# Performance work log

Measured on AMD Instinct MI355X. Metric: run time of the kernel, lower is better.

Reference implementation:

```python
import jax, jax.numpy as jnp
import numpy as np

B, P, ENC = 128, 196, 2048   # batch, num_pixels (14x14), encoder_dim
L, V = 50, 10000             # max caption length, vocab
A, D, E = 512, 512, 512      # attention_dim, decoder_dim, embed_dim


def setup_inputs() -> dict:
    key = jax.random.key(0)
    ks = jax.random.split(key, 24)
    def nrm(k, shape, s=0.02):
        return jax.random.normal(k, shape, jnp.float32) * s
    def uni(k, shape, lim=0.1):
        return jax.random.uniform(k, shape, jnp.float32, -lim, lim)
    cap_len = jax.random.randint(ks[2], (B,), 2, L + 1).at[0].set(L)  # ensure max dec_len = L-1 (static)
    return {
        "encoder_out": jax.random.normal(ks[0], (B, P, ENC), jnp.float32),
        "enc_cap": jax.random.randint(ks[1], (B, L), 0, V),
        "cap_len": cap_len,
        "emb_W": uni(ks[3], (V, E)),
        "init_h_W": nrm(ks[4], (D, ENC)), "init_h_b": jnp.zeros((D,), jnp.float32),
        "init_c_W": nrm(ks[5], (D, ENC)), "init_c_b": jnp.zeros((D,), jnp.float32),
        "enc_attn_W": nrm(ks[6], (A, ENC)), "enc_attn_b": jnp.zeros((A,), jnp.float32),
        "dec_attn_W": nrm(ks[7], (A, D)), "dec_attn_b": jnp.zeros((A,), jnp.float32),
        "full_attn_W": nrm(ks[8], (1, A)), "full_attn_b": jnp.zeros((1,), jnp.float32),
        "lstm_Wih": nrm(ks[9], (4 * D, E + ENC)), "lstm_Whh": nrm(ks[10], (4 * D, D)),
        "lstm_bih": jnp.zeros((4 * D,), jnp.float32), "lstm_bhh": jnp.zeros((4 * D,), jnp.float32),
        "fbeta_W": nrm(ks[11], (ENC, D)), "fbeta_b": jnp.zeros((ENC,), jnp.float32),
        "fc_W": uni(ks[12], (V, D)), "fc_b": jnp.zeros((V,), jnp.float32),
    }


def _forward(encoder_out, enc_cap, cap_len,
             emb_W, init_h_W, init_h_b, init_c_W, init_c_b,
             enc_attn_W, enc_attn_b, dec_attn_W, dec_attn_b,
             full_attn_W, full_attn_b, lstm_Wih, lstm_Whh, lstm_bih, lstm_bhh,
             fbeta_W, fbeta_b, fc_W, fc_b):
    Bsz, Pn, Ed = encoder_out.shape
    Dd = lstm_Whh.shape[1]
    # sort by decreasing length (stable, like torch.sort)
    sort_ind = jnp.argsort(-cap_len, stable=True)
    cap_sorted = cap_len[sort_ind]
    dec_len = cap_sorted - 1                       # [B]
    enc_s = encoder_out[sort_ind]                  # [B,P,ENC]
    caps_s = enc_cap[sort_ind]                     # [B,L]
    emb = emb_W[caps_s]                            # [B,L,E]
    enc_mean = enc_s.mean(axis=1)
    h0 = enc_mean @ init_h_W.T + init_h_b
    c0 = enc_mean @ init_c_W.T + init_c_b
    # precompute encoder attention features once (done per-step in torch, same values)
    enc_feat = jnp.einsum('bpe,ae->bpa', enc_s, enc_attn_W) + enc_attn_b  # [B,P,A]
    T = enc_cap.shape[1] - 1                       # static max decode steps

    def step(carry, t):
        h, c = carry
        active = (dec_len > t)[:, None].astype(h.dtype)         # [B,1]
        dec_feat = h @ dec_attn_W.T + dec_attn_b                # [B,A]
        attn = jax.nn.relu(enc_feat + dec_feat[:, None, :])     # [B,P,A]
        scores = attn @ full_attn_W[0] + full_attn_b[0]         # [B,P]
        alpha = jax.nn.softmax(scores, axis=1)                  # [B,P]
        ctx = jnp.einsum('bpe,bp->be', enc_s, alpha)            # [B,ENC]
        gate = jax.nn.sigmoid(h @ fbeta_W.T + fbeta_b)          # [B,ENC]
        ctx = gate * ctx
        x = jnp.concatenate([emb[:, t, :], ctx], axis=1)        # [B,E+ENC]
        gates = x @ lstm_Wih.T + lstm_bih + h @ lstm_Whh.T + lstm_bhh
        i_g, f_g, g_g, o_g = jnp.split(gates, 4, axis=1)
        c_new = jax.nn.sigmoid(f_g) * c + jax.nn.sigmoid(i_g) * jnp.tanh(g_g)
        h_new = jax.nn.sigmoid(o_g) * jnp.tanh(c_new)
        # dropout is identity in eval mode
        out = (h_new @ fc_W.T + fc_b) * active                  # zero rows past dec_len
        alpha = alpha * active
        # freeze state for finished sequences (matches torch's h[:bs] slicing)
        h = active * h_new + (1.0 - active) * h
        c = active * c_new + (1.0 - active) * c
        return (h, c), (out, alpha)

    (_, _), (outs, alphas) = jax.lax.scan(step, (h0, c0), jnp.arange(T))
    output = jnp.swapaxes(outs, 0, 1)    # [B,T,V]
    alphas = jnp.swapaxes(alphas, 0, 1)  # [B,T,P]
    return output, caps_s, dec_len, alphas, sort_ind


def reference(encoder_out, enc_cap, cap_len,
              emb_W, init_h_W, init_h_b, init_c_W, init_c_b,
              enc_attn_W, enc_attn_b, dec_attn_W, dec_attn_b,
              full_attn_W, full_attn_b, lstm_Wih, lstm_Whh, lstm_bih, lstm_bhh,
              fbeta_W, fbeta_b, fc_W, fc_b):
    return _forward(encoder_out, enc_cap, cap_len,
                    emb_W, init_h_W, init_h_b, init_c_W, init_c_b,
                    enc_attn_W, enc_attn_b, dec_attn_W, dec_attn_b,
                    full_attn_W, full_attn_b, lstm_Wih, lstm_Whh, lstm_bih, lstm_bhh,
                    fbeta_W, fbeta_b, fc_W, fc_b)
```

## Files before the change

### kernel.cpp

```cpp
#include <hip/hip_runtime.h>
#include <hip/hip_bf16.h>

#define B_    128
#define P_    196
#define ENCD  2048
#define LL    50
#define VV    10000
#define AA    512
#define DD    512
#define EE    512
#define TT    49
#define XKK   3072
#define PROJN 2560
#define VPAD  10048

#define OUT0_OFF 0
#define OUT1_OFF 62720000
#define OUT2_OFF 62726400
#define OUT3_OFF 62726528
#define OUT4_OFF 63955840

#define WS_SI      0ull
#define WS_DLEN    512ull
#define WS_BATTN   1024ull
// ... 31 lines not shown
__device__ __forceinline__ void gload_lds16(const void* g, void* l) {
    __builtin_amdgcn_global_load_lds((const __attribute__((address_space(1))) void*)g,
                                     (__attribute__((address_space(3))) void*)l, 16, 0, 0);
}

__global__ void sort_kernel(const int* __restrict__ cap_len, const int* __restrict__ enc_cap,
                            int* __restrict__ si, int* __restrict__ dlen,
                            float* __restrict__ out_caps, float* __restrict__ out_dlen,
                            float* __restrict__ out_sind)
{
    __shared__ int cl[B_];
    __shared__ int rank_to_idx[B_];
    int i = threadIdx.x;
    cl[i] = cap_len[i];
    __syncthreads();
    int my = cl[i];
    int r = 0;
    for (int j = 0; j < B_; ++j) {
        int oj = cl[j];
        if (oj > my || (oj == my && j < i)) ++r;
    }
    rank_to_idx[r] = i;
    __syncthreads();
    int src = rank_to_idx[i];
    si[i] = src;
    int dl = cl[src] - 1;
    dlen[i] = dl;
    out_dlen[i] = (float)dl;
    out_sind[i] = (float)src;
    for (int k = 0; k < LL; ++k) out_caps[i * LL + k] = (float)enc_cap[src * LL + k];
}

__global__ void bias_cat_kernel(const float* __restrict__ dec_b, const float* __restrict__ fbeta_b,
                                const float* __restrict__ bih, const float* __restrict__ bhh,
                                float* __restrict__ b_attn, float* __restrict__ b_lstm)
{
    int i = blockIdx.x * 256 + threadIdx.x;
    if (i < AA) b_attn[i] = dec_b[i];
    else if (i < PROJN) b_attn[i] = fbeta_b[i - AA];
    if (i < 2048) b_lstm[i] = bih[i] + bhh[i];
}

__global__ void enc_mean_sorted(const float* __restrict__ enc, const int* __restrict__ si,
                                float* __restrict__ means)
{
    int idx = blockIdx.x * 256 + threadIdx.x;
    int b = idx >> 11, e = idx & 2047;
    const float* p = enc + (size_t)si[b] * P_ * ENCD + e;
    float s = 0.f;
    for (int q = 0; q < P_; ++q) s += p[(size_t)q * ENCD];
    means[idx] = s * (1.0f / 196.0f);
}

template<int MODE, bool CONV, int BK2>
__launch_bounds__(256)
__global__ void mfma_gemm(const void* __restrict__ Av, const void* __restrict__ Wv,
                          const float* __restrict__ bias, const int* __restrict__ dlen,
                          float* __restrict__ Cf, unsigned short* __restrict__ Cbf,
                          int K, int KC, long long ldc, long long slabStride, int Nreal)
{
    constexpr int RB = BK2 * 2;
    constexpr int AL = (128 * RB) / 4096;
    constexpr int WL = (64 * RB) / 4096;
    __shared__ __align__(16) unsigned short As[2][128 * BK2];
    __shared__ __align__(16) unsigned short Ws[2][64 * BK2];
    const int tid  = threadIdx.x;
    const int wave = tid >> 6, lane = tid & 63;
    const int m0 = (MODE == 2 ? blockIdx.x : blockIdx.y) * 128;
    const int n0 = (MODE == 2 ? blockIdx.y : blockIdx.x) * 64;
    const int z  = blockIdx.z;
    const int kbeg = z * KC;
    const int nt = KC / BK2;
    const int r16 = lane & 15, kg = lane >> 4;

    f32x4 acc[8];
    #pragma unroll
    for (int i = 0; i < 8; ++i) acc[i] = f32x4{0.f, 0.f, 0.f, 0.f};

    const int c_arow = tid >> 1, c_acb = (tid & 1) * 16;
    const int c_wrow = tid >> 2, c_wcb = (tid & 3) * 8;

    int buf = 0;

    if constexpr (!CONV) {
        const unsigned short* A = (const unsigned short*)Av;
        const unsigned short* W = (const unsigned short*)Wv;
        #pragma unroll
        for (int s = 0; s < AL; ++s) {
            int L = s * 4096 + wave * 1024 + lane * 16;
            gload_lds16(A + (size_t)(m0 + L / RB) * K + kbeg + (L % RB) / 2,
                        &As[0][(s * 4096 + wave * 1024) / 2]);
        }
        #pragma unroll
        for (int s = 0; s < WL; ++s) {
            int L = s * 4096 + wave * 1024 + lane * 16;
            gload_lds16(W + (size_t)(n0 + L / RB) * K + kbeg + (L % RB) / 2,
                        &Ws[0][(s * 4096 + wave * 1024) / 2]);
        }
        __syncthreads();
        for (int it = 0; it < nt; ++it) {
            if (it + 1 < nt) {
                int k1 = kbeg + (it + 1) * BK2;
                #pragma unroll
                for (int s = 0; s < AL; ++s) {
                    int L = s * 4096 + wave * 1024 + lane * 16;
                    gload_lds16(A + (size_t)(m0 + L / RB) * K + k1 + (L % RB) / 2,
                                &As[buf ^ 1][(s * 4096 + wave * 1024) / 2]);
                }
                #pragma unroll
                for (int s = 0; s < WL; ++s) {
                    int L = s * 4096 + wave * 1024 + lane * 16;
                    gload_lds16(W + (size_t)(n0 + L / RB) * K + k1 + (L % RB) / 2,
                                &Ws[buf ^ 1][(s * 4096 + wave * 1024) / 2]);
                }
            }
            #pragma unroll
            for (int kk2 = 0; kk2 < BK2 / 32; ++kk2) {
                s16x8 bfrag = *(const s16x8*)&Ws[buf][(wave * 16 + r16) * BK2 + kk2 * 32 + kg * 8];
                #pragma unroll
                for (int i = 0; i < 8; ++i) {
                    s16x8 afrag = *(const s16x8*)&As[buf][(i * 16 + r16) * BK2 + kk2 * 32 + kg * 8];
                    acc[i] = __builtin_amdgcn_mfma_f32_16x16x32_bf16(afrag, bfrag, acc[i], 0, 0, 0);
                }
            }
            __syncthreads();
            buf ^= 1;
        }
    } else {
        static_assert(!CONV || BK2 == 32, "CONV path requires BK2==32");
        const float* A = (const float*)Av;
        const float* W = (const float*)Wv;
        float ra[16], rw[8];
        #pragma unroll
        for (int j = 0; j < 16; ++j) ra[j] = A[(size_t)(m0 + c_arow) * K + kbeg + c_acb + j];
        #pragma unroll
        for (int j = 0; j < 8; ++j)  rw[j] = W[(size_t)(n0 + c_wrow) * K + kbeg + c_wcb + j];
        {
            unsigned short t0[16], t1[8];
            #pragma unroll
            for (int j = 0; j < 16; ++j) t0[j] = f2bf(ra[j]);
            #pragma unroll
            for (int j = 0; j < 8; ++j)  t1[j] = f2bf(rw[j]);
            *(s16x8*)&As[0][c_arow * 32 + c_acb]     = *(s16x8*)&t0[0];
            *(s16x8*)&As[0][c_arow * 32 + c_acb + 8] = *(s16x8*)&t0[8];
            *(s16x8*)&Ws[0][c_wrow * 32 + c_wcb]     = *(s16x8*)&t1[0];
        }
        __syncthreads();
        for (int it = 0; it < nt; ++it) {
            float ra2[16], rw2[8];
            bool more = (it + 1 < nt);
            if (more) {
                int k1 = kbeg + (it + 1) * 32;
                #pragma unroll
                for (int j = 0; j < 16; ++j) ra2[j] = A[(size_t)(m0 + c_arow) * K + k1 + c_acb + j];
                #pragma unroll
                for (int j = 0; j < 8; ++j)  rw2[j] = W[(size_t)(n0 + c_wrow) * K + k1 + c_wcb + j];
            }
            s16x8 bfrag = *(const s16x8*)&Ws[buf][(wave * 16 + r16) * 32 + kg * 8];
            #pragma unroll
            for (int i = 0; i < 8; ++i) {
                s16x8 afrag = *(const s16x8*)&As[buf][(i * 16 + r16) * 32 + kg * 8];
                acc[i] = __builtin_amdgcn_mfma_f32_16x16x32_bf16(afrag, bfrag, acc[i], 0, 0, 0);
            }
            if (more) {
                unsigned short t0[16], t1[8];
                #pragma unroll
                for (int j = 0; j < 16; ++j) t0[j] = f2bf(ra2[j]);
                #pragma unroll
                for (int j = 0; j < 8; ++j)  t1[j] = f2bf(rw2[j]);
                *(s16x8*)&As[buf ^ 1][c_arow * 32 + c_acb]     = *(s16x8*)&t0[0];
                *(s16x8*)&As[buf ^ 1][c_arow * 32 + c_acb + 8] = *(s16x8*)&t0[8];
                *(s16x8*)&Ws[buf ^ 1][c_wrow * 32 + c_wcb]     = *(s16x8*)&t1[0];
            }
            __syncthreads();
            buf ^= 1;
        }
    }

    int n = n0 + wave * 16 + r16;
    float bv = 0.f;
    if (bias && z == 0) bv = (MODE == 2) ? (n < Nreal ? bias[n] : 0.f) : bias[n];
    float* Cz = Cf + (size_t)z * slabStride;
    #pragma unroll
    for (int i = 0; i < 8; ++i) {
        #pragma unroll
        for (int r = 0; r < 4; ++r) {
            int m = m0 + i * 16 + kg * 4 + r;
            float v = acc[i][r] + bv;
            if (MODE == 0) {
                Cz[(size_t)m * ldc + n] = v;
            } else if (MODE == 1) {
                Cbf[(size_t)m * ldc + n] = f2bf(v);
            } else {
                int bb = m & 127, tt2 = m >> 7;
                if (n < Nreal)
                    Cf[((size_t)bb * TT + tt2) * VV + n] = (dlen[bb] > tt2) ? v : 0.f;
            }
        }
    }
}

template<int NS>
__global__ void attn_kernel(const unsigned short* __restrict__ efeat,
                            const float* __restrict__ proj, const float* __restrict__ battn,
                            const float* __restrict__ full_W, const float* __restrict__ full_b,
                            const int* __restrict__ si, const int* __restrict__ dlen,
                            const int* __restrict__ enc_cap, const float* __restrict__ emb_W,
                            const unsigned short* __restrict__ h_bf,
                            const unsigned short* __restrict__ encbf,
                            const float* __restrict__ encf, int use_bf,
                            float* __restrict__ alphas_out, unsigned short* __restrict__ xcat, int t)
{
    int b = blockIdx.y, x = blockIdx.x, tid = threadIdx.x;
    int wave = tid >> 6, lane = tid & 63;
    bool active = dlen[b] > t;
    if (!active) {
        if (x == 0 && tid < P_) alphas_out[((size_t)b * TT + t) * P_ + tid] = 0.f;
        return;
    }
    __shared__ float df[AA];
    __shared__ float wf[AA];
    __shared__ float sal[P_];
    __shared__ float red[8];
    const float* pz = proj + (size_t)b * PROJN;
    const size_t ps = (size_t)B_ * PROJN;
    for (int i = tid; i < AA; i += 256) {
        float v = battn[i];
        #pragma unroll
        for (int z = 0; z < NS; ++z) v += pz[z * ps + i];
        df[i] = v; wf[i] = full_W[i];
    }
    __syncthreads();
    int sb = si[b];
    float s = full_b[0];
    if (tid < P_) {
        const unsigned short* ef = efeat + ((size_t)sb * P_ + tid) * AA;
        #pragma unroll 8
        for (int e8 = 0; e8 < 64; ++e8) {
            s16x8 ev = *(const s16x8*)(ef + e8 * 8);
            #pragma unroll
            for (int j = 0; j < 8; ++j) {
                float v = bf2f((unsigned short)ev[j]) + df[e8 * 8 + j];
                v = v > 0.f ? v : 0.f;
                s = fmaf(v, wf[e8 * 8 + j], s);
            }
        }
    }
    float v = (tid < P_) ? s : -1e30f;
    float m = v;
    #pragma unroll
    for (int off = 32; off; off >>= 1) m = fmaxf(m, __shfl_down(m, off));
// ... 8 lines not shown
    for (int off = 32; off; off >>= 1) ssum += __shfl_down(ssum, off);
    if (lane == 0) red[wave] = ssum;
    __syncthreads();
    if (tid == 0) red[5] = 1.0f / (red[0] + red[1] + red[2] + red[3]);
    __syncthreads();
    float al = e * red[5];
    if (tid < P_) sal[tid] = al;
    if (x == 0) {
        if (tid < P_) alphas_out[((size_t)b * TT + t) * P_ + tid] = al;
        int tok = enc_cap[sb * LL + t];
        for (int k = tid; k < EE; k += 256) {
            xcat[(size_t)b * XKK + k]        = f2bf(emb_W[(size_t)tok * EE + k]);
            xcat[(size_t)b * XKK + 2560 + k] = h_bf[b * DD + k];
        }
    }
    __syncthreads();

    int e0 = x * 1024 + tid * 4;
    float a0 = 0.f, a1 = 0.f, a2 = 0.f, a3 = 0.f;
    if (use_bf) {
        const unsigned short* base = encbf + (size_t)sb * P_ * ENCD + e0;
        #pragma unroll 7
        for (int p = 0; p < P_; ++p) {
            uint2 u = *(const uint2*)(base + (size_t)p * ENCD);
            float alp = sal[p];
            a0 = fmaf(alp, __uint_as_float(u.x << 16), a0);
            a1 = fmaf(alp, __uint_as_float(u.x & 0xffff0000u), a1);
            a2 = fmaf(alp, __uint_as_float(u.y << 16), a2);
            a3 = fmaf(alp, __uint_as_float(u.y & 0xffff0000u), a3);
        }
    } else {
        const float* base = encf + (size_t)sb * P_ * ENCD + e0;
        #pragma unroll 7
        for (int p = 0; p < P_; ++p) {
            float4 u = *(const float4*)(base + (size_t)p * ENCD);
            float alp = sal[p];
            a0 = fmaf(alp, u.x, a0); a1 = fmaf(alp, u.y, a1);
            a2 = fmaf(alp, u.z, a2); a3 = fmaf(alp, u.w, a3);
        }
    }
    int ei = AA + e0;
    float4 gl = *(const float4*)&battn[ei];
    #pragma unroll
    for (int z = 0; z < NS; ++z) {
        float4 gp = *(const float4*)&pz[z * ps + ei];
        gl.x += gp.x; gl.y += gp.y; gl.z += gp.z; gl.w += gp.w;
    }
    ushort4 xo;
    xo.x = f2bf(a0 * sigmoidf_(gl.x));
    xo.y = f2bf(a1 * sigmoidf_(gl.y));
    xo.z = f2bf(a2 * sigmoidf_(gl.z));
    xo.w = f2bf(a3 * sigmoidf_(gl.w));
    *(ushort4*)&xcat[(size_t)b * XKK + EE + e0] = xo;
}

template<int NS>
__global__ void pointwise_kernel(const float* __restrict__ gates, const float* __restrict__ blstm,
                                 const int* __restrict__ dlen,
                                 float* __restrict__ h, float* __restrict__ c,
                                 unsigned short* __restrict__ h_bf, unsigned short* __restrict__ hstore,
                                 int t)
{
    int idx = blockIdx.x * 256 + threadIdx.x;
    int b = idx >> 9, d = idx & 511;
    bool act = dlen[b] > (t - 1);
    if (!act) {
        hstore[((size_t)(t - 1) * B_ + b) * DD + d] = 0;
        return;
    }
    const size_t slab = (size_t)B_ * 2048;
    const float* g = gates + (size_t)b * 2048;
    float gi = blstm[d], gf = blstm[512 + d], gg = blstm[1024 + d], go = blstm[1536 + d];
    #pragma unroll
    for (int z = 0; z < NS; ++z) {
        gi += g[z * slab + d];
        gf += g[z * slab + 512 + d];
        gg += g[z * slab + 1024 + d];
        go += g[z * slab + 1536 + d];
    }
    float cn = sigmoidf_(gf) * c[idx] + sigmoidf_(gi) * tanhf(gg);
    float hn = sigmoidf_(go) * tanhf(cn);
    unsigned short hb = f2bf(hn);
    hstore[((size_t)(t - 1) * B_ + b) * DD + d] = hb;
    h[idx] = hn; c[idx] = cn;
    h_bf[idx] = hb;
}

__global__ void conv_bf16_kernel(const float* __restrict__ src, unsigned short* __restrict__ dst, int n4)
{
    for (int i = blockIdx.x * 256 + threadIdx.x; i < n4; i += gridDim.x * 256) {
        float4 v = ((const float4*)src)[i];
        ushort4 o;
        o.x = f2bf(v.x); o.y = f2bf(v.y); o.z = f2bf(v.z); o.w = f2bf(v.w);
        ((ushort4*)dst)[i] = o;
    }
}
__global__ void conv_wproj_kernel(const float* __restrict__ dec_W, const float* __restrict__ fbeta_W,
                                  unsigned short* __restrict__ dst)
{
    int k = blockIdx.x * 256 + threadIdx.x, n = blockIdx.y;
    float v = (n < AA) ? dec_W[(size_t)n * DD + k] : fbeta_W[(size_t)(n - AA) * DD + k];
    dst[(size_t)n * DD + k] = f2bf(v);
}
__global__ void conv_wcat_kernel(const float* __restrict__ Wih, const float* __restrict__ Whh,
                                 unsigned short* __restrict__ dst)
{
    int k = blockIdx.x * 256 + threadIdx.x, n = blockIdx.y;
    float v = (k < 2560) ? Wih[(size_t)n * 2560 + k] : Whh[(size_t)n * DD + (k - 2560)];
    dst[(size_t)n * XKK + k] = f2bf(v);
}
__global__ void conv_fcw_kernel(const float* __restrict__ fc_W, unsigned short* __restrict__ dst)
{
    int k = blockIdx.x * 256 + threadIdx.x, n = blockIdx.y;
    float v = (n < VV) ? fc_W[(size_t)n * DD + k] : 0.f;
    dst[(size_t)n * DD + k] = f2bf(v);
}

extern "C" void kernel_launch(void* const* d_in, const int* in_sizes, int n_in,
                              void* d_out, int out_size, void* d_ws, size_t ws_size,
                              hipStream_t stream)
{
    const float* encoder_out = (const float*)d_in[0];
    const int*   enc_cap     = (const int*)d_in[1];
    const int*   cap_len     = (const int*)d_in[2];
    const float* emb_W       = (const float*)d_in[3];
    const float* init_h_W    = (const float*)d_in[4];
    const float* init_h_b    = (const float*)d_in[5];
    const float* init_c_W    = (const float*)d_in[6];
    const float* init_c_b    = (const float*)d_in[7];
    const float* enc_attn_W  = (const float*)d_in[8];
    const float* enc_attn_b  = (const float*)d_in[9];
    const float* dec_attn_W  = (const float*)d_in[10];
    const float* dec_attn_b  = (const float*)d_in[11];
    const float* full_attn_W = (const float*)d_in[12];
    const float* full_attn_b = (const float*)d_in[13];
    const float* lstm_Wih    = (const float*)d_in[14];
    const float* lstm_Whh    = (const float*)d_in[15];
    const float* lstm_bih    = (const float*)d_in[16];
    const float* lstm_bhh    = (const float*)d_in[17];
    const float* fbeta_W     = (const float*)d_in[18];
    const float* fbeta_b     = (const float*)d_in[19];
    const float* fc_W        = (const float*)d_in[20];
    const float* fc_b        = (const float*)d_in[21];

    char* wsb = (char*)d_ws;
    int*   si     = (int*)(wsb + WS_SI);
    int*   dlen   = (int*)(wsb + WS_DLEN);
    float* battn  = (float*)(wsb + WS_BATTN);
    float* blstm  = (float*)(wsb + WS_BLSTM);
    float* means  = (float*)(wsb + WS_MEANS);
    float* h      = (float*)(wsb + WS_H);
    float* c      = (float*)(wsb + WS_C);
    unsigned short* h_bf   = (unsigned short*)(wsb + WS_HBF);
    float* proj   = (float*)(wsb + WS_PROJ);
    unsigned short* xcat   = (unsigned short*)(wsb + WS_XCAT);
    float* gates  = (float*)(wsb + WS_GATES);
    unsigned short* hstore = (unsigned short*)(wsb + WS_HSTORE);
    unsigned short* wproj  = (unsigned short*)(wsb + WS_WPROJ);
    unsigned short* wcat   = (unsigned short*)(wsb + WS_WCAT);
    unsigned short* fcw    = (unsigned short*)(wsb + WS_FCW);
    unsigned short* wenc   = (unsigned short*)(wsb + WS_WENC);
    unsigned short* efeat  = (unsigned short*)(wsb + WS_EFEAT);
    unsigned short* encbf  = (unsigned short*)(wsb + WS_ENCBF);

    float* out      = (float*)d_out;
    float* out0     = out + OUT0_OFF;
    float* out_caps = out + OUT1_OFF;
    float* out_dlen = out + OUT2_OFF;
    float* alphas   = out + OUT3_OFF;
    float* out_sind = out + OUT4_OFF;

    const int use_encbf = (ws_size >= NEED_ENCBF) ? 1 : 0;

    sort_kernel<<<1, B_, 0, stream>>>(cap_len, enc_cap, si, dlen, out_caps, out_dlen, out_sind);
    bias_cat_kernel<<<10, 256, 0, stream>>>(dec_attn_b, fbeta_b, lstm_bih, lstm_bhh, battn, blstm);
    enc_mean_sorted<<<(B_ * ENCD) / 256, 256, 0, stream>>>(encoder_out, si, means);

    mfma_gemm<0, true, 32><<<dim3(DD / 64, 1, 1), 256, 0, stream>>>(
        means, init_h_W, init_h_b, nullptr, h, nullptr, ENCD, ENCD, DD, 0, DD);
    mfma_gemm<0, true, 32><<<dim3(DD / 64, 1, 1), 256, 0, stream>>>(
        means, init_c_W, init_c_b, nullptr, c, nullptr, ENCD, ENCD, DD, 0, DD);
    conv_bf16_kernel<<<64, 256, 0, stream>>>(h, h_bf, (B_ * DD) / 4);

    conv_wproj_kernel<<<dim3(2, PROJN), 256, 0, stream>>>(dec_attn_W, fbeta_W, wproj);
    conv_wcat_kernel<<<dim3(12, 2048), 256, 0, stream>>>(lstm_Wih, lstm_Whh, wcat);
    conv_fcw_kernel<<<dim3(2, VPAD), 256, 0, stream>>>(fc_W, fcw);
    conv_bf16_kernel<<<256, 256, 0, stream>>>(enc_attn_W, wenc, (AA * ENCD) / 4);
    if (use_encbf)
        conv_bf16_kernel<<<2048, 256, 0, stream>>>(encoder_out, encbf, (B_ * P_ * ENCD) / 4);

    if (use_encbf)
        mfma_gemm<1, false, 64><<<dim3(AA / 64, (B_ * P_) / 128, 1), 256, 0, stream>>>(
            encbf, wenc, enc_attn_b, nullptr, nullptr, efeat, ENCD, ENCD, AA, 0, AA);
    else
        mfma_gemm<1, true, 32><<<dim3(AA / 64, (B_ * P_) / 128, 1), 256, 0, stream>>>(
            encoder_out, enc_attn_W, enc_attn_b, nullptr, nullptr, efeat, ENCD, ENCD, AA, 0, AA);

    for (int t = 0; t < TT; ++t) {
        if (t > 0)
            pointwise_kernel<8><<<(B_ * DD) / 256, 256, 0, stream>>>(
                gates, blstm, dlen, h, c, h_bf, hstore, t);

        mfma_gemm<0, false, 64><<<dim3(PROJN / 64, 1, 4), 256, 0, stream>>>(
            h_bf, wproj, nullptr, nullptr, proj, nullptr, DD, 128, PROJN, (long long)B_ * PROJN, PROJN);

        attn_kernel<4><<<dim3(2, B_), 256, 0, stream>>>(
            efeat, proj, battn, full_attn_W, full_attn_b, si, dlen, enc_cap, emb_W, h_bf,
            encbf, encoder_out, use_encbf, alphas, xcat, t);

        mfma_gemm<0, false, 64><<<dim3(2048 / 64, 1, 8), 256, 0, stream>>>(
            xcat, wcat, nullptr, nullptr, gates, nullptr, XKK, 384, 2048, (long long)B_ * 2048, 2048);
    }
    pointwise_kernel<8><<<(B_ * DD) / 256, 256, 0, stream>>>(
        gates, blstm, dlen, h, c, h_bf, hstore, TT);

    mfma_gemm<2, false, 64><<<dim3(TT, VPAD / 64, 1), 256, 0, stream>>>(
        hstore, fcw, fc_b, dlen, out0, nullptr, DD, DD, VV, 0, VV);
}
```

Baseline: 2.973 ms.

## Fuse LSTM pointwise into gates GEMM via last-block counter; weight-stationary FC

Folds the per-step LSTM pointwise update into the gates GEMM kernel. Each group of 32 blocks covering one 64-column slice bumps an atomic counter, and the last block to arrive runs the cell update for that slice, which removes one kernel launch per timestep. The final vocab projection becomes a dedicated kernel that keeps a 64-row slice of the FC weights resident in LDS and loops over all timesteps, avoiding repeated weight loads. The counter reuses the means workspace slot after means is consumed, and the fused path depends on correct fences and monotonic counter targets across steps.

```diff
diff --git a/kernel.cpp b/kernel.cpp
--- a/kernel.cpp
+++ b/kernel.cpp
@@ -107,6 +107,12 @@
     means[idx] = s * (1.0f / 196.0f);
 }
 
+__global__ void zero_gcnt_kernel(unsigned int* gcnt)
+{
+    if (threadIdx.x < 8)
+        __hip_atomic_store(&gcnt[threadIdx.x * 32], 0u, __ATOMIC_RELEASE, __HIP_MEMORY_SCOPE_AGENT);
+}
+
 template<int MODE, bool CONV, int BK2>
 __launch_bounds__(256)
 __global__ void mfma_gemm(const void* __restrict__ Av, const void* __restrict__ Wv,
@@ -121,8 +127,8 @@
     __shared__ __align__(16) unsigned short Ws[2][64 * BK2];
     const int tid  = threadIdx.x;
     const int wave = tid >> 6, lane = tid & 63;
-    const int m0 = (MODE == 2 ? blockIdx.x : blockIdx.y) * 128;
-    const int n0 = (MODE == 2 ? blockIdx.y : blockIdx.x) * 64;
+    const int m0 = blockIdx.y * 128;
+    const int n0 = blockIdx.x * 64;
     const int z  = blockIdx.z;
     const int kbeg = z * KC;
     const int nt = KC / BK2;
@@ -233,8 +239,7 @@
     }
 
     int n = n0 + wave * 16 + r16;
-    float bv = 0.f;
-    if (bias && z == 0) bv = (MODE == 2) ? (n < Nreal ? bias[n] : 0.f) : bias[n];
+    float bv = (bias && z == 0) ? bias[n] : 0.f;
     float* Cz = Cf + (size_t)z * slabStride;
     #pragma unroll
     for (int i = 0; i < 8; ++i) {
@@ -242,14 +247,196 @@
         for (int r = 0; r < 4; ++r) {
             int m = m0 + i * 16 + kg * 4 + r;
             float v = acc[i][r] + bv;
-            if (MODE == 0) {
-                Cz[(size_t)m * ldc + n] = v;
-            } else if (MODE == 1) {
-                Cbf[(size_t)m * ldc + n] = f2bf(v);
-            } else {
-                int bb = m & 127, tt2 = m >> 7;
-                if (n < Nreal)
-                    Cf[((size_t)bb * TT + tt2) * VV + n] = (dlen[bb] > tt2) ? v : 0.f;
+            if (MODE == 0) Cz[(size_t)m * ldc + n] = v;
+            else           Cbf[(size_t)m * ldc + n] = f2bf(v);
+        }
+    }
+}
+
+__launch_bounds__(256)
+__global__ void gates_pw_kernel(const unsigned short* __restrict__ Axc,
+                                const unsigned short* __restrict__ Wc,
+                                float* __restrict__ gates, const float* __restrict__ blstm,
+                                const int* __restrict__ dlen,
+                                float* __restrict__ h, float* __restrict__ c,
+                                unsigned short* __restrict__ h_bf, unsigned short* __restrict__ hstore,
+                                unsigned int* __restrict__ gcnt, int t)
+{
+    constexpr int BK2 = 64, RB = 128, AL = 4, WL = 2, NT = 6;
+    __shared__ __align__(16) unsigned short As[2][128 * BK2];
+    __shared__ __align__(16) unsigned short Ws[2][64 * BK2];
+    __shared__ int slast;
+    const int tid  = threadIdx.x;
+    const int wave = tid >> 6, lane = tid & 63;
+    const int ntile = blockIdx.x;
+    const int z  = blockIdx.z;
+    const int n0 = ntile * 64;
+    const int kbeg = z * 384;
+    const int r16 = lane & 15, kg = lane >> 4;
+
+    f32x4 acc[8];
+    #pragma unroll
+    for (int i = 0; i < 8; ++i) acc[i] = f32x4{0.f, 0.f, 0.f, 0.f};
+
+    int buf = 0;
+    #pragma unroll
+    for (int s = 0; s < AL; ++s) {
+        int L = s * 4096 + wave * 1024 + lane * 16;
+        gload_lds16(Axc + (size_t)(L / RB) * XKK + kbeg + (L % RB) / 2,
+                    &As[0][(s * 4096 + wave * 1024) / 2]);
+    }
+    #pragma unroll
+    for (int s = 0; s < WL; ++s) {
+        int L = s * 4096 + wave * 1024 + lane * 16;
+        gload_lds16(Wc + (size_t)(n0 + L / RB) * XKK + kbeg + (L % RB) / 2,
+                    &Ws[0][(s * 4096 + wave * 1024) / 2]);
+    }
+    __syncthreads();
+    for (int it = 0; it < NT; ++it) {
+        if (it + 1 < NT) {
+            int k1 = kbeg + (it + 1) * BK2;
+            #pragma unroll
+            for (int s = 0; s < AL; ++s) {
+                int L = s * 4096 + wave * 1024 + lane * 16;
+                gload_lds16(Axc + (size_t)(L / RB) * XKK + k1 + (L % RB) / 2,
+                            &As[buf ^ 1][(s * 4096 + wave * 1024) / 2]);
+            }
+            #pragma unroll
+            for (int s = 0; s < WL; ++s) {
+                int L = s * 4096 + wave * 1024 + lane * 16;
+                gload_lds16(Wc + (size_t)(n0 + L / RB) * XKK + k1 + (L % RB) / 2,
+                            &Ws[buf ^ 1][(s * 4096 + wave * 1024) / 2]);
+            }
+        }
+        #pragma unroll
+        for (int kk2 = 0; kk2 < 2; ++kk2) {
+            s16x8 bfrag = *(const s16x8*)&Ws[buf][(wave * 16 + r16) * BK2 + kk2 * 32 + kg * 8];
+            #pragma unroll
+            for (int i = 0; i < 8; ++i) {
+                s16x8 afrag = *(const s16x8*)&As[buf][(i * 16 + r16) * BK2 + kk2 * 32 + kg * 8];
+                acc[i] = __builtin_amdgcn_mfma_f32_16x16x32_bf16(afrag, bfrag, acc[i], 0, 0, 0);
+            }
+        }
+        __syncthreads();
+        buf ^= 1;
+    }
+    int n = n0 + wave * 16 + r16;
+    float* Cz = gates + (size_t)z * B_ * 2048;
+    #pragma unroll
+    for (int i = 0; i < 8; ++i)
+        #pragma unroll
+        for (int r = 0; r < 4; ++r)
+            Cz[(size_t)(i * 16 + kg * 4 + r) * 2048 + n] = acc[i][r];
+
+    int g = ntile & 7;
+    __syncthreads();
+    if (tid == 0) {
+        __threadfence();
+        unsigned int old = __hip_atomic_fetch_add(&gcnt[g * 32], 1u,
+                                __ATOMIC_ACQ_REL, __HIP_MEMORY_SCOPE_AGENT);
+        int last = (old == 32u * (unsigned)(t + 1) - 1u);
+        if (last) __threadfence();
+        slast = last;
+    }
+    __syncthreads();
+    if (slast) {
+        const size_t slab = (size_t)B_ * 2048;
+        for (int i = tid; i < B_ * 64; i += 256) {
+            int b = i >> 6, d = (g << 6) + (i & 63);
+            bool act = dlen[b] > t;
+            if (!act) {
+                hstore[((size_t)t * B_ + b) * DD + d] = 0;
+                continue;
+            }
+            const float* gg0 = gates + (size_t)b * 2048;
+            float gi = blstm[d], gf = blstm[512 + d];
+            float gG = blstm[1024 + d], go = blstm[1536 + d];
+            #pragma unroll
+            for (int z2 = 0; z2 < 8; ++z2) {
+                const float* gz = gg0 + z2 * slab;
+                gi += gz[d];
+                gf += gz[512 + d];
+                gG += gz[1024 + d];
+                go += gz[1536 + d];
+            }
+            int idx = (b << 9) + d;
+            float cn = sigmoidf_(gf) * c[idx] + sigmoidf_(gi) * tanhf(gG);
+            float hn = sigmoidf_(go) * tanhf(cn);
+            unsigned short hb = f2bf(hn);
+            hstore[((size_t)t * B_ + b) * DD + d] = hb;
+            h[idx] = hn; c[idx] = cn;
+            h_bf[idx] = hb;
+        }
+    }
+}
+
+__launch_bounds__(256, 1)
+__global__ void fc_kernel(const unsigned short* __restrict__ hstore,
+                          const unsigned short* __restrict__ fcw,
+                          const float* __restrict__ fc_b, const int* __restrict__ dlen,
+                          float* __restrict__ out0)
+{
+    __shared__ __align__(16) unsigned short WsF[64 * 512];
+    __shared__ __align__(16) unsigned short As[2][128 * 64];
+    const int tid = threadIdx.x, wave = tid >> 6, lane = tid & 63;
+    const int n0 = blockIdx.x * 64;
+    const int r16 = lane & 15, kg = lane >> 4;
+
+    #pragma unroll
+    for (int s = 0; s < 16; ++s) {
+        int L = s * 4096 + wave * 1024 + lane * 16;
+        gload_lds16(fcw + (size_t)(n0 + L / 1024) * DD + (L % 1024) / 2,
+                    &WsF[(s * 4096 + wave * 1024) / 2]);
+    }
+
+    int n = n0 + wave * 16 + r16;
+    float bv = (n < VV) ? fc_b[n] : 0.f;
+
+    #pragma unroll 1
+    for (int mt = 0; mt < TT; ++mt) {
+        const int m0 = mt * 128;
+        f32x4 acc[8];
+        #pragma unroll
+        for (int i = 0; i < 8; ++i) acc[i] = f32x4{0.f, 0.f, 0.f, 0.f};
+        int buf = 0;
+        #pragma unroll
+        for (int s = 0; s < 4; ++s) {
+            int L = s * 4096 + wave * 1024 + lane * 16;
+            gload_lds16(hstore + (size_t)(m0 + L / 128) * DD + (L % 128) / 2,
+                        &As[0][(s * 4096 + wave * 1024) / 2]);
+        }
+        __syncthreads();
+        for (int it = 0; it < 8; ++it) {
+            if (it + 1 < 8) {
+                int k1 = (it + 1) * 64;
+                #pragma unroll
+                for (int s = 0; s < 4; ++s) {
+                    int L = s * 4096 + wave * 1024 + lane * 16;
+                    gload_lds16(hstore + (size_t)(m0 + L / 128) * DD + k1 + (L % 128) / 2,
+                                &As[buf ^ 1][(s * 4096 + wave * 1024) / 2]);
+                }
+            }
+            #pragma unroll
+            for (int kk2 = 0; kk2 < 2; ++kk2) {
+                int k0 = it * 64 + kk2 * 32;
+                s16x8 bfrag = *(const s16x8*)&WsF[(wave * 16 + r16) * DD + k0 + kg * 8];
+                #pragma unroll
+                for (int i = 0; i < 8; ++i) {
+                    s16x8 afrag = *(const s16x8*)&As[buf][(i * 16 + r16) * 64 + kk2 * 32 + kg * 8];
+                    acc[i] = __builtin_amdgcn_mfma_f32_16x16x32_bf16(afrag, bfrag, acc[i], 0, 0, 0);
+                }
+            }
+            __syncthreads();
+            buf ^= 1;
+        }
+        if (n < VV) {
+            #pragma unroll
+            for (int i = 0; i < 8; ++i) {
+                #pragma unroll
+                for (int r = 0; r < 4; ++r) {
+                    int b = i * 16 + kg * 4 + r;
+                    out0[((size_t)b * TT + mt) * VV + n] = (dlen[b] > mt) ? acc[i][r] + bv : 0.f;
+                }
             }
         }
     }
@@ -366,38 +553,6 @@
     xo.z = f2bf(a2 * sigmoidf_(gl.z));
     xo.w = f2bf(a3 * sigmoidf_(gl.w));
     *(ushort4*)&xcat[(size_t)b * XKK + EE + e0] = xo;
-}
-
-template<int NS>
-__global__ void pointwise_kernel(const float* __restrict__ gates, const float* __restrict__ blstm,
-                                 const int* __restrict__ dlen,
-                                 float* __restrict__ h, float* __restrict__ c,
-                                 unsigned short* __restrict__ h_bf, unsigned short* __restrict__ hstore,
-                                 int t)
-{
-    int idx = blockIdx.x * 256 + threadIdx.x;
-    int b = idx >> 9, d = idx & 511;
-    bool act = dlen[b] > (t - 1);
-    if (!act) {
-        hstore[((size_t)(t - 1) * B_ + b) * DD + d] = 0;
-        return;
-    }
-    const size_t slab = (size_t)B_ * 2048;
-    const float* g = gates + (size_t)b * 2048;
-    float gi = blstm[d], gf = blstm[512 + d], gg = blstm[1024 + d], go = blstm[1536 + d];
-    #pragma unroll
-    for (int z = 0; z < NS; ++z) {
-        gi += g[z * slab + d];
-        gf += g[z * slab + 512 + d];
-        gg += g[z * slab + 1024 + d];
-        go += g[z * slab + 1536 + d];
-    }
-    float cn = sigmoidf_(gf) * c[idx] + sigmoidf_(gi) * tanhf(gg);
-    float hn = sigmoidf_(go) * tanhf(cn);
-    unsigned short hb = f2bf(hn);
-    hstore[((size_t)(t - 1) * B_ + b) * DD + d] = hb;
-    h[idx] = hn; c[idx] = cn;
-    h_bf[idx] = hb;
 }
 
 __global__ void conv_bf16_kernel(const float* __restrict__ src, unsigned short* __restrict__ dst, int n4)
@@ -463,6 +618,7 @@
     float* battn  = (float*)(wsb + WS_BATTN);
     float* blstm  = (float*)(wsb + WS_BLSTM);
     float* means  = (float*)(wsb + WS_MEANS);
+    unsigned int* gcnt = (unsigned int*)(wsb + WS_MEANS);
     float* h      = (float*)(wsb + WS_H);
     float* c      = (float*)(wsb + WS_C);
     unsigned short* h_bf   = (unsigned short*)(wsb + WS_HBF);
@@ -495,6 +651,7 @@
     mfma_gemm<0, true, 32><<<dim3(DD / 64, 1, 1), 256, 0, stream>>>(
         means, init_c_W, init_c_b, nullptr, c, nullptr, ENCD, ENCD, DD, 0, DD);
     conv_bf16_kernel<<<64, 256, 0, stream>>>(h, h_bf, (B_ * DD) / 4);
+    zero_gcnt_kernel<<<1, 64, 0, stream>>>(gcnt);
 
     conv_wproj_kernel<<<dim3(2, PROJN), 256, 0, stream>>>(dec_attn_W, fbeta_W, wproj);
     conv_wcat_kernel<<<dim3(12, 2048), 256, 0, stream>>>(lstm_Wih, lstm_Whh, wcat);
@@ -511,10 +668,6 @@
             encoder_out, enc_attn_W, enc_attn_b, nullptr, nullptr, efeat, ENCD, ENCD, AA, 0, AA);
 
     for (int t = 0; t < TT; ++t) {
-        if (t > 0)
-            pointwise_kernel<8><<<(B_ * DD) / 256, 256, 0, stream>>>(
-                gates, blstm, dlen, h, c, h_bf, hstore, t);
-
         mfma_gemm<0, false, 64><<<dim3(PROJN / 64, 1, 4), 256, 0, stream>>>(
             h_bf, wproj, nullptr, nullptr, proj, nullptr, DD, 128, PROJN, (long long)B_ * PROJN, PROJN);
 
@@ -522,12 +675,9 @@
             efeat, proj, battn, full_attn_W, full_attn_b, si, dlen, enc_cap, emb_W, h_bf,
             encbf, encoder_out, use_encbf, alphas, xcat, t);
 
-        mfma_gemm<0, false, 64><<<dim3(2048 / 64, 1, 8), 256, 0, stream>>>(
-            xcat, wcat, nullptr, nullptr, gates, nullptr, XKK, 384, 2048, (long long)B_ * 2048, 2048);
-    }
-    pointwise_kernel<8><<<(B_ * DD) / 256, 256, 0, stream>>>(
-        gates, blstm, dlen, h, c, h_bf, hstore, TT);
-
-    mfma_gemm<2, false, 64><<<dim3(TT, VPAD / 64, 1), 256, 0, stream>>>(
-        hstore, fcw, fc_b, dlen, out0, nullptr, DD, DD, VV, 0, VV);
-}
+        gates_pw_kernel<<<dim3(32, 1, 8), 256, 0, stream>>>(
+            xcat, wcat, gates, blstm, dlen, h, c, h_bf, hstore, gcnt, t);
+    }
+
+    fc_kernel<<<dim3(VPAD / 64), 256, 0, stream>>>(hstore, fcw, fc_b, dlen, out0);
+}
```

New measurement: 4.702 ms. 58.1% more time.

## XOR-swizzle LDS tiles and add dedicated FC kernel with resident weight slab

Applied to the files above, without the earlier changes.

The generic MFMA GEMM now XOR-swizzles the column offset of its BK=64 shared-memory tiles, both when loading and when reading fragments, to avoid LDS bank conflicts. The final vocab projection gets its own kernel. Each block keeps a full 64x512 slab of fc weights in LDS and loops over 7 time-step tiles of hidden states, reusing the weights instead of reloading them per tile. This cuts global weight traffic and bank conflicts, but the large LDS footprint and launch_bounds(256,1) limit occupancy, and the grid is smaller.

```diff
diff --git a/kernel.cpp b/kernel.cpp
--- a/kernel.cpp
+++ b/kernel.cpp
@@ -117,16 +117,18 @@
     constexpr int RB = BK2 * 2;
     constexpr int AL = (128 * RB) / 4096;
     constexpr int WL = (64 * RB) / 4096;
+    constexpr bool SW = (BK2 == 64);
     __shared__ __align__(16) unsigned short As[2][128 * BK2];
     __shared__ __align__(16) unsigned short Ws[2][64 * BK2];
     const int tid  = threadIdx.x;
     const int wave = tid >> 6, lane = tid & 63;
-    const int m0 = (MODE == 2 ? blockIdx.x : blockIdx.y) * 128;
-    const int n0 = (MODE == 2 ? blockIdx.y : blockIdx.x) * 64;
+    const int m0 = blockIdx.y * 128;
+    const int n0 = blockIdx.x * 64;
     const int z  = blockIdx.z;
     const int kbeg = z * KC;
     const int nt = KC / BK2;
     const int r16 = lane & 15, kg = lane >> 4;
+    const int swz = SW ? ((r16 & 7) << 3) : 0;
 
     f32x4 acc[8];
     #pragma unroll
@@ -143,13 +145,17 @@
         #pragma unroll
         for (int s = 0; s < AL; ++s) {
             int L = s * 4096 + wave * 1024 + lane * 16;
-            gload_lds16(A + (size_t)(m0 + L / RB) * K + kbeg + (L % RB) / 2,
+            int row = L / RB;
+            int col = (L % RB) ^ (SW ? ((row & 7) << 4) : 0);
+            gload_lds16(A + (size_t)(m0 + row) * K + kbeg + col / 2,
                         &As[0][(s * 4096 + wave * 1024) / 2]);
         }
         #pragma unroll
         for (int s = 0; s < WL; ++s) {
             int L = s * 4096 + wave * 1024 + lane * 16;
-            gload_lds16(W + (size_t)(n0 + L / RB) * K + kbeg + (L % RB) / 2,
+            int row = L / RB;
+            int col = (L % RB) ^ (SW ? ((row & 7) << 4) : 0);
+            gload_lds16(W + (size_t)(n0 + row) * K + kbeg + col / 2,
                         &Ws[0][(s * 4096 + wave * 1024) / 2]);
         }
         __syncthreads();
@@ -159,22 +165,26 @@
                 #pragma unroll
                 for (int s = 0; s < AL; ++s) {
                     int L = s * 4096 + wave * 1024 + lane * 16;
-                    gload_lds16(A + (size_t)(m0 + L / RB) * K + k1 + (L % RB) / 2,
+                    int row = L / RB;
+                    int col = (L % RB) ^ (SW ? ((row & 7) << 4) : 0);
+                    gload_lds16(A + (size_t)(m0 + row) * K + k1 + col / 2,
                                 &As[buf ^ 1][(s * 4096 + wave * 1024) / 2]);
                 }
                 #pragma unroll
                 for (int s = 0; s < WL; ++s) {
                     int L = s * 4096 + wave * 1024 + lane * 16;
-                    gload_lds16(W + (size_t)(n0 + L / RB) * K + k1 + (L % RB) / 2,
+                    int row = L / RB;
+                    int col = (L % RB) ^ (SW ? ((row & 7) << 4) : 0);
+                    gload_lds16(W + (size_t)(n0 + row) * K + k1 + col / 2,
                                 &Ws[buf ^ 1][(s * 4096 + wave * 1024) / 2]);
                 }
             }
             #pragma unroll
             for (int kk2 = 0; kk2 < BK2 / 32; ++kk2) {
-                s16x8 bfrag = *(const s16x8*)&Ws[buf][(wave * 16 + r16) * BK2 + kk2 * 32 + kg * 8];
+                s16x8 bfrag = *(const s16x8*)&Ws[buf][(wave * 16 + r16) * BK2 + ((kk2 * 32 + kg * 8) ^ swz)];
                 #pragma unroll
                 for (int i = 0; i < 8; ++i) {
-                    s16x8 afrag = *(const s16x8*)&As[buf][(i * 16 + r16) * BK2 + kk2 * 32 + kg * 8];
+                    s16x8 afrag = *(const s16x8*)&As[buf][(i * 16 + r16) * BK2 + ((kk2 * 32 + kg * 8) ^ swz)];
                     acc[i] = __builtin_amdgcn_mfma_f32_16x16x32_bf16(afrag, bfrag, acc[i], 0, 0, 0);
                 }
             }
@@ -233,8 +243,7 @@
     }
 
     int n = n0 + wave * 16 + r16;
-    float bv = 0.f;
-    if (bias && z == 0) bv = (MODE == 2) ? (n < Nreal ? bias[n] : 0.f) : bias[n];
+    float bv = (bias && z == 0) ? bias[n] : 0.f;
     float* Cz = Cf + (size_t)z * slabStride;
     #pragma unroll
     for (int i = 0; i < 8; ++i) {
@@ -242,14 +251,87 @@
         for (int r = 0; r < 4; ++r) {
             int m = m0 + i * 16 + kg * 4 + r;
             float v = acc[i][r] + bv;
-            if (MODE == 0) {
-                Cz[(size_t)m * ldc + n] = v;
-            } else if (MODE == 1) {
-                Cbf[(size_t)m * ldc + n] = f2bf(v);
-            } else {
-                int bb = m & 127, tt2 = m >> 7;
-                if (n < Nreal)
-                    Cf[((size_t)bb * TT + tt2) * VV + n] = (dlen[bb] > tt2) ? v : 0.f;
+            if (MODE == 0) Cz[(size_t)m * ldc + n] = v;
+            else           Cbf[(size_t)m * ldc + n] = f2bf(v);
+        }
+    }
+}
+
+__launch_bounds__(256, 1)
+__global__ void fc_kernel(const unsigned short* __restrict__ hstore,
+                          const unsigned short* __restrict__ fcw,
+                          const float* __restrict__ fc_b, const int* __restrict__ dlen,
+                          float* __restrict__ out0)
+{
+    __shared__ __align__(16) unsigned short WsF[64 * 512];
+    __shared__ __align__(16) unsigned short As[2][128 * 64];
+    const int tid = threadIdx.x, wave = tid >> 6, lane = tid & 63;
+    const int n0 = blockIdx.x * 64;
+    const int r16 = lane & 15, kg = lane >> 4;
+    const int swz = (r16 & 7) << 3;
+
+    #pragma unroll
+    for (int s = 0; s < 16; ++s) {
+        int L = s * 4096 + wave * 1024 + lane * 16;
+        int row = L >> 10;
+        int col = (L & 1023) ^ ((row & 7) << 4);
+        gload_lds16(fcw + (size_t)(n0 + row) * DD + (col >> 1),
+                    &WsF[(s * 4096 + wave * 1024) / 2]);
+    }
+
+    int n = n0 + wave * 16 + r16;
+    float bv = (n < VV) ? fc_b[n] : 0.f;
+
+    #pragma unroll 1
+    for (int j = 0; j < 7; ++j) {
+        const int mt = blockIdx.y * 7 + j;
+        const int m0 = mt * 128;
+        f32x4 acc[8];
+        #pragma unroll
+        for (int i = 0; i < 8; ++i) acc[i] = f32x4{0.f, 0.f, 0.f, 0.f};
+        int buf = 0;
+        #pragma unroll
+        for (int s = 0; s < 4; ++s) {
+            int L = s * 4096 + wave * 1024 + lane * 16;
+            int row = L >> 7;
+            int col = (L & 127) ^ ((row & 7) << 4);
+            gload_lds16(hstore + (size_t)(m0 + row) * DD + (col >> 1),
+                        &As[0][(s * 4096 + wave * 1024) / 2]);
+        }
+        __syncthreads();
+        for (int it = 0; it < 8; ++it) {
+            if (it + 1 < 8) {
+                int k1 = (it + 1) * 64;
+                #pragma unroll
+                for (int s = 0; s < 4; ++s) {
+                    int L = s * 4096 + wave * 1024 + lane * 16;
+                    int row = L >> 7;
+                    int col = (L & 127) ^ ((row & 7) << 4);
+                    gload_lds16(hstore + (size_t)(m0 + row) * DD + k1 + (col >> 1),
+                                &As[buf ^ 1][(s * 4096 + wave * 1024) / 2]);
+                }
+            }
+            #pragma unroll
+            for (int kk2 = 0; kk2 < 2; ++kk2) {
+                int k0 = it * 64 + kk2 * 32;
+                s16x8 bfrag = *(const s16x8*)&WsF[(wave * 16 + r16) * DD + ((k0 + kg * 8) ^ swz)];
+                #pragma unroll
+                for (int i = 0; i < 8; ++i) {
+                    s16x8 afrag = *(const s16x8*)&As[buf][(i * 16 + r16) * 64 + ((kk2 * 32 + kg * 8) ^ swz)];
+                    acc[i] = __builtin_amdgcn_mfma_f32_16x16x32_bf16(afrag, bfrag, acc[i], 0, 0, 0);
+                }
+            }
+            __syncthreads();
+            buf ^= 1;
+        }
+        if (n < VV) {
+            #pragma unroll
+            for (int i = 0; i < 8; ++i) {
+                #pragma unroll
+                for (int r = 0; r < 4; ++r) {
+                    int b = i * 16 + kg * 4 + r;
+                    out0[((size_t)b * TT + mt) * VV + n] = (dlen[b] > mt) ? acc[i][r] + bv : 0.f;
+                }
             }
         }
     }
@@ -528,6 +610,5 @@
     pointwise_kernel<8><<<(B_ * DD) / 256, 256, 0, stream>>>(
         gates, blstm, dlen, h, c, h_bf, hstore, TT);
 
-    mfma_gemm<2, false, 64><<<dim3(TT, VPAD / 64, 1), 256, 0, stream>>>(
-        hstore, fcw, fc_b, dlen, out0, nullptr, DD, DD, VV, 0, VV);
-}
+    fc_kernel<<<dim3(VPAD / 64, 7), 256, 0, stream>>>(hstore, fcw, fc_b, dlen, out0);
+}
```

Result: no change. 2.964 ms (-0.3%).

## Fuse LSTM gate GEMM with pointwise cell update and swizzle LDS tiles

Applied to the files above, without the earlier changes.

Replaces the split-K gate GEMM (8 slabs of fp32 partials) plus a separate pointwise kernel with one fused kernel per step. The gate weight rows are permuted so each 64-column tile holds all four gates for 16 hidden units, letting the tile finish the LSTM cell update in registers/LDS. This removes the partial-sum round trip and one launch per step, but the fused kernel runs only 32 blocks each covering the full 3072 K, cutting parallelism. It also adds an XOR swizzle to the LDS layout for BK2=64 GEMMs to reduce bank conflicts.

```diff
diff --git a/kernel.cpp b/kernel.cpp
--- a/kernel.cpp
+++ b/kernel.cpp
@@ -117,6 +117,7 @@
     constexpr int RB = BK2 * 2;
     constexpr int AL = (128 * RB) / 4096;
     constexpr int WL = (64 * RB) / 4096;
+    constexpr bool SW = (BK2 == 64);
     __shared__ __align__(16) unsigned short As[2][128 * BK2];
     __shared__ __align__(16) unsigned short Ws[2][64 * BK2];
     const int tid  = threadIdx.x;
@@ -127,6 +128,7 @@
     const int kbeg = z * KC;
     const int nt = KC / BK2;
     const int r16 = lane & 15, kg = lane >> 4;
+    const int swz = SW ? ((r16 & 7) << 3) : 0;
 
     f32x4 acc[8];
     #pragma unroll
@@ -143,13 +145,17 @@
         #pragma unroll
         for (int s = 0; s < AL; ++s) {
             int L = s * 4096 + wave * 1024 + lane * 16;
-            gload_lds16(A + (size_t)(m0 + L / RB) * K + kbeg + (L % RB) / 2,
+            int row = L / RB;
+            int col = (L % RB) ^ (SW ? ((row & 7) << 4) : 0);
+            gload_lds16(A + (size_t)(m0 + row) * K + kbeg + col / 2,
                         &As[0][(s * 4096 + wave * 1024) / 2]);
         }
         #pragma unroll
         for (int s = 0; s < WL; ++s) {
             int L = s * 4096 + wave * 1024 + lane * 16;
-            gload_lds16(W + (size_t)(n0 + L / RB) * K + kbeg + (L % RB) / 2,
+            int row = L / RB;
+            int col = (L % RB) ^ (SW ? ((row & 7) << 4) : 0);
+            gload_lds16(W + (size_t)(n0 + row) * K + kbeg + col / 2,
                         &Ws[0][(s * 4096 + wave * 1024) / 2]);
         }
         __syncthreads();
@@ -159,22 +165,26 @@
                 #pragma unroll
                 for (int s = 0; s < AL; ++s) {
                     int L = s * 4096 + wave * 1024 + lane * 16;
-                    gload_lds16(A + (size_t)(m0 + L / RB) * K + k1 + (L % RB) / 2,
+                    int row = L / RB;
+                    int col = (L % RB) ^ (SW ? ((row & 7) << 4) : 0);
+                    gload_lds16(A + (size_t)(m0 + row) * K + k1 + col / 2,
                                 &As[buf ^ 1][(s * 4096 + wave * 1024) / 2]);
                 }
                 #pragma unroll
                 for (int s = 0; s < WL; ++s) {
                     int L = s * 4096 + wave * 1024 + lane * 16;
-                    gload_lds16(W + (size_t)(n0 + L / RB) * K + k1 + (L % RB) / 2,
+                    int row = L / RB;
+                    int col = (L % RB) ^ (SW ? ((row & 7) << 4) : 0);
+                    gload_lds16(W + (size_t)(n0 + row) * K + k1 + col / 2,
                                 &Ws[buf ^ 1][(s * 4096 + wave * 1024) / 2]);
                 }
             }
             #pragma unroll
             for (int kk2 = 0; kk2 < BK2 / 32; ++kk2) {
-                s16x8 bfrag = *(const s16x8*)&Ws[buf][(wave * 16 + r16) * BK2 + kk2 * 32 + kg * 8];
+                s16x8 bfrag = *(const s16x8*)&Ws[buf][(wave * 16 + r16) * BK2 + ((kk2 * 32 + kg * 8) ^ swz)];
                 #pragma unroll
                 for (int i = 0; i < 8; ++i) {
-                    s16x8 afrag = *(const s16x8*)&As[buf][(i * 16 + r16) * BK2 + kk2 * 32 + kg * 8];
+                    s16x8 afrag = *(const s16x8*)&As[buf][(i * 16 + r16) * BK2 + ((kk2 * 32 + kg * 8) ^ swz)];
                     acc[i] = __builtin_amdgcn_mfma_f32_16x16x32_bf16(afrag, bfrag, acc[i], 0, 0, 0);
                 }
             }
@@ -252,6 +262,109 @@
                     Cf[((size_t)bb * TT + tt2) * VV + n] = (dlen[bb] > tt2) ? v : 0.f;
             }
         }
+    }
+}
+
+__launch_bounds__(256)
+__global__ void gates_fused_kernel(const unsigned short* __restrict__ Axc,
+                                   const unsigned short* __restrict__ Wc,
+                                   const float* __restrict__ blstm, const int* __restrict__ dlen,
+                                   float* __restrict__ h, float* __restrict__ c,
+                                   unsigned short* __restrict__ h_bf,
+                                   unsigned short* __restrict__ hstore, int t)
+{
+    constexpr int BK2 = 64, RB = 128, AL = 4, WL = 2, NT = XKK / BK2;
+    __shared__ __align__(16) unsigned short smem[2 * 128 * BK2 + 2 * 64 * BK2];
+    unsigned short (*As)[128 * BK2] = (unsigned short(*)[128 * BK2])smem;
+    unsigned short (*Ws)[64 * BK2]  = (unsigned short(*)[64 * BK2])(smem + 2 * 128 * BK2);
+    const int tid  = threadIdx.x;
+    const int wave = tid >> 6, lane = tid & 63;
+    const int ntile = blockIdx.x;
+    const int n0 = ntile * 64;
+    const int r16 = lane & 15, kg = lane >> 4;
+    const int swz = (r16 & 7) << 3;
+
+    f32x4 acc[8];
+    #pragma unroll
+    for (int i = 0; i < 8; ++i) acc[i] = f32x4{0.f, 0.f, 0.f, 0.f};
+
+    int buf = 0;
+    #pragma unroll
+    for (int s = 0; s < AL; ++s) {
+        int L = s * 4096 + wave * 1024 + lane * 16;
+        int row = L / RB;
+        int col = (L % RB) ^ ((row & 7) << 4);
+        gload_lds16(Axc + (size_t)row * XKK + col / 2, &As[0][(s * 4096 + wave * 1024) / 2]);
+    }
+    #pragma unroll
+    for (int s = 0; s < WL; ++s) {
+        int L = s * 4096 + wave * 1024 + lane * 16;
+        int row = L / RB;
+        int col = (L % RB) ^ ((row & 7) << 4);
+        gload_lds16(Wc + (size_t)(n0 + row) * XKK + col / 2, &Ws[0][(s * 4096 + wave * 1024) / 2]);
+    }
+    __syncthreads();
+    for (int it = 0; it < NT; ++it) {
+        if (it + 1 < NT) {
+            int k1 = (it + 1) * BK2;
+            #pragma unroll
+            for (int s = 0; s < AL; ++s) {
+                int L = s * 4096 + wave * 1024 + lane * 16;
+                int row = L / RB;
+                int col = (L % RB) ^ ((row & 7) << 4);
+                gload_lds16(Axc + (size_t)row * XKK + k1 + col / 2,
+                            &As[buf ^ 1][(s * 4096 + wave * 1024) / 2]);
+            }
+            #pragma unroll
+            for (int s = 0; s < WL; ++s) {
+                int L = s * 4096 + wave * 1024 + lane * 16;
+                int row = L / RB;
+                int col = (L % RB) ^ ((row & 7) << 4);
+                gload_lds16(Wc + (size_t)(n0 + row) * XKK + k1 + col / 2,
+                            &Ws[buf ^ 1][(s * 4096 + wave * 1024) / 2]);
+            }
+        }
+        #pragma unroll
+        for (int kk2 = 0; kk2 < 2; ++kk2) {
+            s16x8 bfrag = *(const s16x8*)&Ws[buf][(wave * 16 + r16) * BK2 + ((kk2 * 32 + kg * 8) ^ swz)];
+            #pragma unroll
+            for (int i = 0; i < 8; ++i) {
+                s16x8 afrag = *(const s16x8*)&As[buf][(i * 16 + r16) * BK2 + ((kk2 * 32 + kg * 8) ^ swz)];
+                acc[i] = __builtin_amdgcn_mfma_f32_16x16x32_bf16(afrag, bfrag, acc[i], 0, 0, 0);
+            }
+        }
+        __syncthreads();
+        buf ^= 1;
+    }
+
+    float* Cs = (float*)smem;
+    int j = wave * 16 + r16;
+    #pragma unroll
+    for (int i = 0; i < 8; ++i)
+        #pragma unroll
+        for (int r = 0; r < 4; ++r)
+            Cs[(i * 16 + kg * 4 + r) * 65 + j] = acc[i][r];
+    __syncthreads();
+
+    const int d0 = ntile * 16;
+    for (int k = tid; k < 2048; k += 256) {
+        int b = k >> 4, dd = k & 15;
+        int d = d0 + dd;
+        if (dlen[b] <= t) {
+            hstore[((size_t)t * B_ + b) * DD + d] = 0;
+            continue;
+        }
+        float gi = Cs[b * 65 + (dd << 2)    ] + blstm[d];
+        float gf = Cs[b * 65 + (dd << 2) + 1] + blstm[512 + d];
+        float gG = Cs[b * 65 + (dd << 2) + 2] + blstm[1024 + d];
+        float go = Cs[b * 65 + (dd << 2) + 3] + blstm[1536 + d];
+        int idx = (b << 9) + d;
+        float cn = sigmoidf_(gf) * c[idx] + sigmoidf_(gi) * tanhf(gG);
+        float hn = sigmoidf_(go) * tanhf(cn);
+        unsigned short hb = f2bf(hn);
+        hstore[((size_t)t * B_ + b) * DD + d] = hb;
+        h[idx] = hn; c[idx] = cn;
+        h_bf[idx] = hb;
     }
 }
 
@@ -368,38 +481,6 @@
     *(ushort4*)&xcat[(size_t)b * XKK + EE + e0] = xo;
 }
 
-template<int NS>
-__global__ void pointwise_kernel(const float* __restrict__ gates, const float* __restrict__ blstm,
-                                 const int* __restrict__ dlen,
-                                 float* __restrict__ h, float* __restrict__ c,
-                                 unsigned short* __restrict__ h_bf, unsigned short* __restrict__ hstore,
-                                 int t)
-{
-    int idx = blockIdx.x * 256 + threadIdx.x;
-    int b = idx >> 9, d = idx & 511;
-    bool act = dlen[b] > (t - 1);
-    if (!act) {
-        hstore[((size_t)(t - 1) * B_ + b) * DD + d] = 0;
-        return;
-    }
-    const size_t slab = (size_t)B_ * 2048;
-    const float* g = gates + (size_t)b * 2048;
-    float gi = blstm[d], gf = blstm[512 + d], gg = blstm[1024 + d], go = blstm[1536 + d];
-    #pragma unroll
-    for (int z = 0; z < NS; ++z) {
-        gi += g[z * slab + d];
-        gf += g[z * slab + 512 + d];
-        gg += g[z * slab + 1024 + d];
-        go += g[z * slab + 1536 + d];
-    }
-    float cn = sigmoidf_(gf) * c[idx] + sigmoidf_(gi) * tanhf(gg);
-    float hn = sigmoidf_(go) * tanhf(cn);
-    unsigned short hb = f2bf(hn);
-    hstore[((size_t)(t - 1) * B_ + b) * DD + d] = hb;
-    h[idx] = hn; c[idx] = cn;
-    h_bf[idx] = hb;
-}
-
 __global__ void conv_bf16_kernel(const float* __restrict__ src, unsigned short* __restrict__ dst, int n4)
 {
     for (int i = blockIdx.x * 256 + threadIdx.x; i < n4; i += gridDim.x * 256) {
@@ -416,12 +497,13 @@
     float v = (n < AA) ? dec_W[(size_t)n * DD + k] : fbeta_W[(size_t)(n - AA) * DD + k];
     dst[(size_t)n * DD + k] = f2bf(v);
 }
-__global__ void conv_wcat_kernel(const float* __restrict__ Wih, const float* __restrict__ Whh,
-                                 unsigned short* __restrict__ dst)
-{
-    int k = blockIdx.x * 256 + threadIdx.x, n = blockIdx.y;
-    float v = (k < 2560) ? Wih[(size_t)n * 2560 + k] : Whh[(size_t)n * DD + (k - 2560)];
-    dst[(size_t)n * XKK + k] = f2bf(v);
+__global__ void conv_wcat_perm_kernel(const float* __restrict__ Wih, const float* __restrict__ Whh,
+                                      unsigned short* __restrict__ dst)
+{
+    int k = blockIdx.x * 256 + threadIdx.x, pn = blockIdx.y;
+    int o = (pn & 3) * 512 + (pn >> 2);
+    float v = (k < 2560) ? Wih[(size_t)o * 2560 + k] : Whh[(size_t)o * DD + (k - 2560)];
+    dst[(size_t)pn * XKK + k] = f2bf(v);
 }
 __global__ void conv_fcw_kernel(const float* __restrict__ fc_W, unsigned short* __restrict__ dst)
 {
@@ -468,7 +550,6 @@
     unsigned short* h_bf   = (unsigned short*)(wsb + WS_HBF);
     float* proj   = (float*)(wsb + WS_PROJ);
     unsigned short* xcat   = (unsigned short*)(wsb + WS_XCAT);
-    float* gates  = (float*)(wsb + WS_GATES);
     unsigned short* hstore = (unsigned short*)(wsb + WS_HSTORE);
     unsigned short* wproj  = (unsigned short*)(wsb + WS_WPROJ);
     unsigned short* wcat   = (unsigned short*)(wsb + WS_WCAT);
@@ -497,7 +578,7 @@
     conv_bf16_kernel<<<64, 256, 0, stream>>>(h, h_bf, (B_ * DD) / 4);
 
     conv_wproj_kernel<<<dim3(2, PROJN), 256, 0, stream>>>(dec_attn_W, fbeta_W, wproj);
-    conv_wcat_kernel<<<dim3(12, 2048), 256, 0, stream>>>(lstm_Wih, lstm_Whh, wcat);
+    conv_wcat_perm_kernel<<<dim3(12, 2048), 256, 0, stream>>>(lstm_Wih, lstm_Whh, wcat);
     conv_fcw_kernel<<<dim3(2, VPAD), 256, 0, stream>>>(fc_W, fcw);
     conv_bf16_kernel<<<256, 256, 0, stream>>>(enc_attn_W, wenc, (AA * ENCD) / 4);
     if (use_encbf)
@@ -511,10 +592,6 @@
             encoder_out, enc_attn_W, enc_attn_b, nullptr, nullptr, efeat, ENCD, ENCD, AA, 0, AA);
 
     for (int t = 0; t < TT; ++t) {
-        if (t > 0)
-            pointwise_kernel<8><<<(B_ * DD) / 256, 256, 0, stream>>>(
-                gates, blstm, dlen, h, c, h_bf, hstore, t);
-
         mfma_gemm<0, false, 64><<<dim3(PROJN / 64, 1, 4), 256, 0, stream>>>(
             h_bf, wproj, nullptr, nullptr, proj, nullptr, DD, 128, PROJN, (long long)B_ * PROJN, PROJN);
 
@@ -522,11 +599,9 @@
             efeat, proj, battn, full_attn_W, full_attn_b, si, dlen, enc_cap, emb_W, h_bf,
             encbf, encoder_out, use_encbf, alphas, xcat, t);
 
-        mfma_gemm<0, false, 64><<<dim3(2048 / 64, 1, 8), 256, 0, stream>>>(
-            xcat, wcat, nullptr, nullptr, gates, nullptr, XKK, 384, 2048, (long long)B_ * 2048, 2048);
-    }
-    pointwise_kernel<8><<<(B_ * DD) / 256, 256, 0, stream>>>(
-        gates, blstm, dlen, h, c, h_bf, hstore, TT);
+        gates_fused_kernel<<<dim3(32), 256, 0, stream>>>(
+            xcat, wcat, blstm, dlen, h, c, h_bf, hstore, t);
+    }
 
     mfma_gemm<2, false, 64><<<dim3(TT, VPAD / 64, 1), 256, 0, stream>>>(
         hstore, fcw, fc_b, dlen, out0, nullptr, DD, DD, VV, 0, VV);
```

After: 3.960 ms. 33.2% more time.
